# Performance work log

Measured on AMD Instinct MI355X. Metric: run time of the kernel, lower is better.

Reference implementation:

```python
import jax, jax.numpy as jnp
import numpy as np

VOCAB = 32000
D_MODEL = 1024
PATCH_LEN = 16
NHEAD = 8
B = 8
S = 4096


def setup_inputs() -> dict:
    key = jax.random.key(0)
    ks = jax.random.split(key, 8)
    token_inputs = jax.random.randint(ks[0], (B, S), 0, VOCAB, dtype=jnp.int64 if jax.config.jax_enable_x64 else jnp.int32)
    attention_mask = jax.random.randint(ks[1], (B, S), 0, 2).astype(bool)
    emb_weight = jax.random.normal(ks[2], (VOCAB, D_MODEL), dtype=jnp.float32) * 0.02
    patch_query = jax.random.normal(ks[3], (1, 1, D_MODEL), dtype=jnp.float32) * 0.02
    # nn.MultiheadAttention packed in-projection [3D, D] and out projection [D, D]
    lim = 1.0 / np.sqrt(D_MODEL)
    in_proj_w = jax.random.uniform(ks[4], (3 * D_MODEL, D_MODEL), jnp.float32, -lim, lim)
    in_proj_b = jnp.zeros((3 * D_MODEL,), jnp.float32)
    out_w = jax.random.uniform(ks[5], (D_MODEL, D_MODEL), jnp.float32, -lim, lim)
    out_b = jnp.zeros((D_MODEL,), jnp.float32)
    return {
        "token_inputs": token_inputs,
        "attention_mask": attention_mask,
        "emb_weight": emb_weight,
        "patch_query": patch_query,
        "in_proj_w": in_proj_w,
        "in_proj_b": in_proj_b,
        "out_w": out_w,
        "out_b": out_b,
    }


def reference(token_inputs, attention_mask, emb_weight, patch_query, in_proj_w, in_proj_b, out_w, out_b):
    d_model = emb_weight.shape[1]
    h, dh = NHEAD, d_model // NHEAD
    L = PATCH_LEN

    tok_emb = emb_weight[token_inputs]              # [B, S, D]
    bsz, seqlen, _ = tok_emb.shape
    # seqlen chosen divisible by PATCH_LEN -> pad_len == 0 (matches torch path)
    num_patches = seqlen // L
    BP = bsz * num_patches
    patch_tokens = tok_emb.reshape(BP, L, d_model)  # [BP, L, D]
    patch_mask = attention_mask.reshape(BP, L)      # True = valid token

    patch_valid = patch_mask.any(axis=1)            # [BP]
    # force position 0 valid for fully-empty patches (safe softmax)
    safe_mask = patch_mask | ((~patch_valid)[:, None] & (jnp.arange(L) == 0)[None, :])

    wq, wk, wv = jnp.split(in_proj_w, 3, axis=0)    # each [D, D]
    bq, bk, bv = jnp.split(in_proj_b, 3, axis=0)

    q = patch_query[0, 0] @ wq.T + bq               # [D] (same query for all patches)
    k = patch_tokens @ wk.T + bk                    # [BP, L, D]
    v = patch_tokens @ wv.T + bv                    # [BP, L, D]

    qh = q.reshape(h, dh)                           # [H, dh]
    kh = k.reshape(BP, L, h, dh)                    # [BP, L, H, dh]
    vh = v.reshape(BP, L, h, dh)

    scale = 1.0 / jnp.sqrt(jnp.asarray(dh, q.dtype))
    scores = jnp.einsum('hd,blhd->bhl', qh, kh) * scale   # [BP, H, L]
    scores = jnp.where(safe_mask[:, None, :], scores, -jnp.inf)
    attn = jax.nn.softmax(scores, axis=-1)                # [BP, H, L]

    ctx = jnp.einsum('bhl,blhd->bhd', attn, vh).reshape(BP, d_model)
    patch_latent = ctx @ out_w.T + out_b                  # [BP, D]

    patch_latent = patch_latent.reshape(bsz, num_patches, d_model)
    pv = patch_valid.reshape(bsz, num_patches)
    patch_latent = patch_latent * pv[..., None].astype(patch_latent.dtype)
    return patch_latent, pv
```

## Files before the change

### kernel.cpp

```cpp
#include <hip/hip_runtime.h>
#include <stdint.h>

#define OUT_LATENT (2048*1024)
#define SCALE 0.08838834764831845f

typedef float f32x4v __attribute__((ext_vector_type(4)));
typedef short s16x8  __attribute__((ext_vector_type(8)));

static __device__ inline unsigned short f2bf(float f) {
    union { float f; uint32_t u; } v; v.f = f;
    uint32_t u = v.u;
    return (unsigned short)((u + 0x7FFFu + ((u >> 16) & 1u)) >> 16);
}
static __device__ inline float bflo(uint32_t u) {
    union { uint32_t u; float f; } v; v.u = u << 16; return v.f;
}
static __device__ inline float bfhi(uint32_t u) {
    union { uint32_t u; float f; } v; v.u = u & 0xFFFF0000u; return v.f;
}

static __device__ __forceinline__ void async16(const unsigned short* g, unsigned short* l) {
    __builtin_amdgcn_global_load_lds(
        (const __attribute__((address_space(1))) void*)g,
        (__attribute__((address_space(3))) void*)l, 16, 0, 0);
}

__global__ __launch_bounds__(256) void k_convw(
    const float* __restrict__ wv_src, const float* __restrict__ ow_src,
    unsigned short* __restrict__ wv_dst, unsigned short* __restrict__ ow_dst) {
    int t = threadIdx.x, b = blockIdx.x;
    const float* src; unsigned short* dst; int idx;
    if (b < 1024) { src = wv_src; dst = wv_dst; idx = b * 1024 + t * 4; }
    else          { src = ow_src; dst = ow_dst; idx = (b - 1024) * 1024 + t * 4; }
    float4 f = *(const float4*)(src + idx);
    ushort4 o; o.x = f2bf(f.x); o.y = f2bf(f.y); o.z = f2bf(f.z); o.w = f2bf(f.w);
    *(ushort4*)(dst + idx) = o;
}

__global__ __launch_bounds__(256) void k_qvec(
    const float* __restrict__ pq, const float* __restrict__ ipw,
    const float* __restrict__ ipb, float* __restrict__ qv) {
    int t = threadIdx.x, wave = t >> 6, lane = t & 63;
    int d = blockIdx.x * 4 + wave;
    const float* wrow = ipw + (size_t)d * 1024;
    float acc = 0.f;
    #pragma unroll
    for (int i = 0; i < 16; ++i) { int j = lane + i * 64; acc = fmaf(pq[j], wrow[j], acc); }
    #pragma unroll
    for (int m = 32; m >= 1; m >>= 1) acc += __shfl_xor(acc, m);
    if (lane == 0) qv[d] = acc + ipb[d];
}

__global__ __launch_bounds__(256) void k_qk(
    const float* __restrict__ qv, const float* __restrict__ ipw,
    const float* __restrict__ ipb, unsigned short* __restrict__ qkb,
    float* __restrict__ sb) {
    __shared__ float qs[128];
    __shared__ float part[128];
    int h = blockIdx.x, jseg = blockIdx.y, t = threadIdx.x;
    int jl = t & 127, dh = t >> 7;
    if (t < 128) qs[t] = qv[h * 128 + t];
    __syncthreads();
    float acc = 0.f;
    const float* wbase = ipw + (size_t)(1024 + h * 128 + dh * 64) * 1024 + jseg * 128 + jl;
    #pragma unroll 8
    for (int d = 0; d < 64; ++d)
        acc = fmaf(qs[dh * 64 + d], wbase[(size_t)d * 1024], acc);
    if (dh) part[jl] = acc;
    __syncthreads();
    if (!dh) qkb[h * 1024 + jseg * 128 + jl] = f2bf((acc + part[jl]) * SCALE);
    if (jseg == 0 && t < 64) {
        const float* bk = ipb + 1024 + h * 128;
        float p = qs[t] * bk[t] + qs[t + 64] * bk[t + 64];
        #pragma unroll
        for (int m = 32; m >= 1; m >>= 1) p += __shfl_xor(p, m);
        if (t == 0) sb[h] = p * SCALE;
    }
}

__global__ __launch_bounds__(256) void k_attn(
    const int* __restrict__ tok_ids, const int* __restrict__ amask,
    const float* __restrict__ emb, const unsigned short* __restrict__ qkb,
    const float* __restrict__ sb, unsigned short* __restrict__ Mout,
    float* __restrict__ pv) {
    __shared__ unsigned short tokL[16][1032];
    __shared__ float scoresP[4][16][8];
    __shared__ float attnL[16][8];
    __shared__ int allzL;

    int bp = blockIdx.x, t = threadIdx.x;
    int wave = t >> 6, lane = t & 63, lrow = lane & 15, quad = lane >> 4;

    s16x8 bfr[8];
    {
        const unsigned short* qbase = qkb + (lane & 7) * 1024 + wave * 256 + quad * 8;
        #pragma unroll
        for (int s = 0; s < 8; ++s) bfr[s] = *(const s16x8*)(qbase + s * 32);
    }

    {
        int row = t >> 4, c = t & 15;
        int tid = tok_ids[bp * 16 + row];
        const float* erow = emb + (size_t)tid * 1024;
        #pragma unroll
        for (int i = 0; i < 16; ++i) {
            int j4 = c + i * 16;
            float4 f = *(const float4*)(erow + j4 * 4);
            ushort4 o; o.x = f2bf(f.x); o.y = f2bf(f.y); o.z = f2bf(f.z); o.w = f2bf(f.w);
            *(ushort4*)(&tokL[row][j4 * 4]) = o;
        }
    }
    if (t < 16) {
        int any = (amask[bp * 16 + t] != 0);
        any |= __shfl_xor(any, 1); any |= __shfl_xor(any, 2);
        any |= __shfl_xor(any, 4); any |= __shfl_xor(any, 8);
        if (t == 0) { pv[bp] = any ? 1.f : 0.f; allzL = any ? 0 : 1; }
    }
    __syncthreads();

    {
        f32x4v acc = (f32x4v){0.f, 0.f, 0.f, 0.f};
        const unsigned short* arow = &tokL[lrow][wave * 256 + quad * 8];
        #pragma unroll
        for (int s = 0; s < 8; ++s) {
            s16x8 af = *(const s16x8*)(arow + s * 32);
            acc = __builtin_amdgcn_mfma_f32_16x16x32_bf16(af, bfr[s], acc, 0, 0, 0);
        }
        if (lrow < 8) {
            #pragma unroll
            for (int r = 0; r < 4; ++r) scoresP[wave][quad * 4 + r][lrow] = acc[r];
        }
    }
    __syncthreads();

    if (t < 128) {
        int hh = t >> 4, ll = t & 15;
        float s = scoresP[0][ll][hh] + scoresP[1][ll][hh]
                + scoresP[2][ll][hh] + scoresP[3][ll][hh] + sb[hh];
        bool valid = (amask[bp * 16 + ll] != 0) || (allzL && ll == 0);
        s = valid ? s : -1e30f;
        float mx = s;
        mx = fmaxf(mx, __shfl_xor(mx, 1)); mx = fmaxf(mx, __shfl_xor(mx, 2));
        mx = fmaxf(mx, __shfl_xor(mx, 4)); mx = fmaxf(mx, __shfl_xor(mx, 8));
        float e = __expf(s - mx);
        float sum = e;
        sum += __shfl_xor(sum, 1); sum += __shfl_xor(sum, 2);
        sum += __shfl_xor(sum, 4); sum += __shfl_xor(sum, 8);
        attnL[ll][hh] = e / sum;
    }
    __syncthreads();

    float macc[8][4];
    #pragma unroll
    for (int h = 0; h < 8; ++h)
        #pragma unroll
        for (int c = 0; c < 4; ++c) macc[h][c] = 0.f;
    #pragma unroll
    for (int ll = 0; ll < 16; ++ll) {
        uint2 tv = *(const uint2*)(&tokL[ll][t * 4]);
        float t0 = bflo(tv.x), t1 = bfhi(tv.x), t2 = bflo(tv.y), t3 = bfhi(tv.y);
        float4 a0 = *(const float4*)(&attnL[ll][0]);
        float4 a1 = *(const float4*)(&attnL[ll][4]);
        macc[0][0] = fmaf(a0.x, t0, macc[0][0]); macc[0][1] = fmaf(a0.x, t1, macc[0][1]);
        macc[0][2] = fmaf(a0.x, t2, macc[0][2]); macc[0][3] = fmaf(a0.x, t3, macc[0][3]);
        macc[1][0] = fmaf(a0.y, t0, macc[1][0]); macc[1][1] = fmaf(a0.y, t1, macc[1][1]);
        macc[1][2] = fmaf(a0.y, t2, macc[1][2]); macc[1][3] = fmaf(a0.y, t3, macc[1][3]);
        macc[2][0] = fmaf(a0.z, t0, macc[2][0]); macc[2][1] = fmaf(a0.z, t1, macc[2][1]);
        macc[2][2] = fmaf(a0.z, t2, macc[2][2]); macc[2][3] = fmaf(a0.z, t3, macc[2][3]);
        macc[3][0] = fmaf(a0.w, t0, macc[3][0]); macc[3][1] = fmaf(a0.w, t1, macc[3][1]);
        macc[3][2] = fmaf(a0.w, t2, macc[3][2]); macc[3][3] = fmaf(a0.w, t3, macc[3][3]);
        macc[4][0] = fmaf(a1.x, t0, macc[4][0]); macc[4][1] = fmaf(a1.x, t1, macc[4][1]);
        macc[4][2] = fmaf(a1.x, t2, macc[4][2]); macc[4][3] = fmaf(a1.x, t3, macc[4][3]);
        macc[5][0] = fmaf(a1.y, t0, macc[5][0]); macc[5][1] = fmaf(a1.y, t1, macc[5][1]);
        macc[5][2] = fmaf(a1.y, t2, macc[5][2]); macc[5][3] = fmaf(a1.y, t3, macc[5][3]);
        macc[6][0] = fmaf(a1.z, t0, macc[6][0]); macc[6][1] = fmaf(a1.z, t1, macc[6][1]);
        macc[6][2] = fmaf(a1.z, t2, macc[6][2]); macc[6][3] = fmaf(a1.z, t3, macc[6][3]);
        macc[7][0] = fmaf(a1.w, t0, macc[7][0]); macc[7][1] = fmaf(a1.w, t1, macc[7][1]);
        macc[7][2] = fmaf(a1.w, t2, macc[7][2]); macc[7][3] = fmaf(a1.w, t3, macc[7][3]);
    }
    #pragma unroll
    for (int h = 0; h < 8; ++h) {
        ushort4 o;
        o.x = f2bf(macc[h][0]); o.y = f2bf(macc[h][1]);
        o.z = f2bf(macc[h][2]); o.w = f2bf(macc[h][3]);
        *(ushort4*)(Mout + ((size_t)(h * 2048 + bp)) * 1024 + t * 4) = o;
    }
}

__device__ __forceinline__ void gemm128_mainloop(
    const unsigned short* __restrict__ A, const unsigned short* __restrict__ B,
    unsigned short* As, unsigned short* Bs, f32x4v acc[4][4]) {
    int t = threadIdx.x;
    int wave = t >> 6, lane = t & 63, lrow = lane & 15, quad = lane >> 4;
    int wm = wave & 1, wn = wave >> 1;
    int srow = t >> 2, sseg = (t & 3) * 8;
    #pragma unroll
    for (int mi = 0; mi < 4; ++mi)
        #pragma unroll
        for (int ni = 0; ni < 4; ++ni) acc[mi][ni] = (f32x4v){0.f, 0.f, 0.f, 0.f};
    for (int step = 0; step < 32; ++step) {
        int k0 = step * 32;
        __syncthreads();
        async16(A + (size_t)srow * 1024 + k0 + sseg,        As + t * 8);
        async16(A + (size_t)(srow + 64) * 1024 + k0 + sseg, As + (256 + t) * 8);
        async16(B + (size_t)srow * 1024 + k0 + sseg,        Bs + t * 8);
        async16(B + (size_t)(srow + 64) * 1024 + k0 + sseg, Bs + (256 + t) * 8);
        __syncthreads();
        s16x8 af[4], bf[4];
        #pragma unroll
        for (int i = 0; i < 4; ++i) {
            af[i] = *(const s16x8*)(As + (wm * 64 + i * 16 + lrow) * 32 + quad * 8);
            bf[i] = *(const s16x8*)(Bs + (wn * 64 + i * 16 + lrow) * 32 + quad * 8);
        }
        #pragma unroll
        for (int mi = 0; mi < 4; ++mi)
            #pragma unroll
            for (int ni = 0; ni < 4; ++ni)
                acc[mi][ni] = __builtin_amdgcn_mfma_f32_16x16x32_bf16(af[mi], bf[ni], acc[mi][ni], 0, 0, 0);
    }
}

__global__ __launch_bounds__(256) void k_gemm_ctx(
    const unsigned short* __restrict__ M, const unsigned short* __restrict__ wv,
    const float* __restrict__ ipb, unsigned short* __restrict__ ctx) {
    __shared__ unsigned short As[128 * 32], Bs[128 * 32];
    int mb = blockIdx.x, h = blockIdx.y;
    f32x4v acc[4][4];
    gemm128_mainloop(M + ((size_t)h * 2048 + mb * 128) * 1024,
                     wv + (size_t)h * 128 * 1024, As, Bs, acc);
    int t = threadIdx.x, wave = t >> 6, lane = t & 63, lrow = lane & 15, quad = lane >> 4;
    int wm = wave & 1, wn = wave >> 1;
    #pragma unroll
    for (int ni = 0; ni < 4; ++ni) {
        int n_g = h * 128 + wn * 64 + ni * 16 + lrow;
        float bias = ipb[2048 + n_g];
        #pragma unroll
        for (int mi = 0; mi < 4; ++mi) {
            #pragma unroll
            for (int r = 0; r < 4; ++r) {
                int m_g = mb * 128 + wm * 64 + mi * 16 + quad * 4 + r;
                ctx[(size_t)m_g * 1024 + n_g] = f2bf(acc[mi][ni][r] + bias);
            }
        }
    }
}

__global__ __launch_bounds__(256) void k_gemm_out(
    const unsigned short* __restrict__ ctx, const unsigned short* __restrict__ ow,
    const float* __restrict__ outb, const float* __restrict__ pv,
    float* __restrict__ out) {
    __shared__ unsigned short As[128 * 32], Bs[128 * 32];
    int mb = blockIdx.x, nb = blockIdx.y;
    f32x4v acc[4][4];
    gemm128_mainloop(ctx + (size_t)mb * 128 * 1024,
                     ow + (size_t)nb * 128 * 1024, As, Bs, acc);
    int t = threadIdx.x, wave = t >> 6, lane = t & 63, lrow = lane & 15, quad = lane >> 4;
    int wm = wave & 1, wn = wave >> 1;
    #pragma unroll
    for (int ni = 0; ni < 4; ++ni) {
        int n_g = nb * 128 + wn * 64 + ni * 16 + lrow;
        float bias = outb[n_g];
        #pragma unroll
        for (int mi = 0; mi < 4; ++mi) {
            #pragma unroll
            for (int r = 0; r < 4; ++r) {
                int m_g = mb * 128 + wm * 64 + mi * 16 + quad * 4 + r;
                out[(size_t)m_g * 1024 + n_g] = (acc[mi][ni][r] + bias) * pv[m_g];
            }
        }
    }
    if (nb == 0 && t < 128) out[OUT_LATENT + mb * 128 + t] = pv[mb * 128 + t];
}

extern "C" void kernel_launch(void* const* d_in, const int* in_sizes, int n_in,
                              void* d_out, int out_size, void* d_ws, size_t ws_size,
                              hipStream_t stream) {
    const int*   tok = (const int*)d_in[0];
    const int*   msk = (const int*)d_in[1];
    const float* emb = (const float*)d_in[2];
    const float* pq  = (const float*)d_in[3];
    const float* ipw = (const float*)d_in[4];
    const float* ipb = (const float*)d_in[5];
    const float* ow  = (const float*)d_in[6];
    const float* ob  = (const float*)d_in[7];
    float* out = (float*)d_out;
    char* ws = (char*)d_ws;

    float*          q_f   = (float*)(ws + 0);
    float*          sb_f  = (float*)(ws + 4096);
    float*          pv_f  = (float*)(ws + 8192);
    unsigned short* qk_b  = (unsigned short*)(ws + 16384);
    unsigned short* wv_b  = (unsigned short*)(ws + 32768);
    unsigned short* ow_b  = (unsigned short*)(ws + 32768 + 2097152);
    unsigned short* ctx_b = (unsigned short*)(ws + 32768 + 2 * 2097152);
    unsigned short* M_b   = (unsigned short*)(ws + 32768 + 2 * 2097152 + 4194304);

    k_convw<<<dim3(2048), dim3(256), 0, stream>>>(ipw + (size_t)2048 * 1024, ow, wv_b, ow_b);
    k_qvec <<<dim3(256),  dim3(256), 0, stream>>>(pq, ipw, ipb, q_f);
    k_qk   <<<dim3(8, 8), dim3(256), 0, stream>>>(q_f, ipw, ipb, qk_b, sb_f);
    k_attn <<<dim3(2048), dim3(256), 0, stream>>>(tok, msk, emb, qk_b, sb_f, M_b, pv_f);
    k_gemm_ctx<<<dim3(16, 8), dim3(256), 0, stream>>>(M_b, wv_b, ipb, ctx_b);
    k_gemm_out<<<dim3(16, 8), dim3(256), 0, stream>>>(ctx_b, ow_b, ob, pv_f, out);
}
```

Baseline: 268.5 us.

## Double-buffer GEMM mainloop, fold weight conversion into attention launch, split qk wider

After: 263.5 us. About the same (-1.9%).

```diff
diff --git a/kernel.cpp b/kernel.cpp
--- a/kernel.cpp
+++ b/kernel.cpp
@@ -23,18 +23,6 @@
     __builtin_amdgcn_global_load_lds(
         (const __attribute__((address_space(1))) void*)g,
         (__attribute__((address_space(3))) void*)l, 16, 0, 0);
-}
-
-__global__ __launch_bounds__(256) void k_convw(
-    const float* __restrict__ wv_src, const float* __restrict__ ow_src,
-    unsigned short* __restrict__ wv_dst, unsigned short* __restrict__ ow_dst) {
-    int t = threadIdx.x, b = blockIdx.x;
-    const float* src; unsigned short* dst; int idx;
-    if (b < 1024) { src = wv_src; dst = wv_dst; idx = b * 1024 + t * 4; }
-    else          { src = ow_src; dst = ow_dst; idx = (b - 1024) * 1024 + t * 4; }
-    float4 f = *(const float4*)(src + idx);
-    ushort4 o; o.x = f2bf(f.x); o.y = f2bf(f.y); o.z = f2bf(f.z); o.w = f2bf(f.w);
-    *(ushort4*)(dst + idx) = o;
 }
 
 __global__ __launch_bounds__(256) void k_qvec(
@@ -56,19 +44,20 @@
     const float* __restrict__ ipb, unsigned short* __restrict__ qkb,
     float* __restrict__ sb) {
     __shared__ float qs[128];
-    __shared__ float part[128];
+    __shared__ float part[3][64];
     int h = blockIdx.x, jseg = blockIdx.y, t = threadIdx.x;
-    int jl = t & 127, dh = t >> 7;
+    int jl = t & 63, dh = t >> 6;
     if (t < 128) qs[t] = qv[h * 128 + t];
     __syncthreads();
     float acc = 0.f;
-    const float* wbase = ipw + (size_t)(1024 + h * 128 + dh * 64) * 1024 + jseg * 128 + jl;
+    const float* wbase = ipw + (size_t)(1024 + h * 128 + dh * 32) * 1024 + jseg * 64 + jl;
     #pragma unroll 8
-    for (int d = 0; d < 64; ++d)
-        acc = fmaf(qs[dh * 64 + d], wbase[(size_t)d * 1024], acc);
-    if (dh) part[jl] = acc;
-    __syncthreads();
-    if (!dh) qkb[h * 1024 + jseg * 128 + jl] = f2bf((acc + part[jl]) * SCALE);
+    for (int d = 0; d < 32; ++d)
+        acc = fmaf(qs[dh * 32 + d], wbase[(size_t)d * 1024], acc);
+    if (dh) part[dh - 1][jl] = acc;
+    __syncthreads();
+    if (!dh) qkb[h * 1024 + jseg * 64 + jl] =
+        f2bf((acc + part[0][jl] + part[1][jl] + part[2][jl]) * SCALE);
     if (jseg == 0 && t < 64) {
         const float* bk = ipb + 1024 + h * 128;
         float p = qs[t] * bk[t] + qs[t + 64] * bk[t + 64];
@@ -78,15 +67,28 @@
     }
 }
 
-__global__ __launch_bounds__(256) void k_attn(
+__global__ __launch_bounds__(256) void k_attn_conv(
     const int* __restrict__ tok_ids, const int* __restrict__ amask,
     const float* __restrict__ emb, const unsigned short* __restrict__ qkb,
     const float* __restrict__ sb, unsigned short* __restrict__ Mout,
-    float* __restrict__ pv) {
+    float* __restrict__ pv,
+    const float* __restrict__ wv_src, const float* __restrict__ ow_src,
+    unsigned short* __restrict__ wv_dst, unsigned short* __restrict__ ow_dst) {
     __shared__ unsigned short tokL[16][1032];
     __shared__ float scoresP[4][16][8];
     __shared__ float attnL[16][8];
     __shared__ int allzL;
+
+    if (blockIdx.x >= 2048) {
+        int b = blockIdx.x - 2048, t = threadIdx.x;
+        const float* src; unsigned short* dst; int idx;
+        if (b < 1024) { src = wv_src; dst = wv_dst; idx = b * 1024 + t * 4; }
+        else          { src = ow_src; dst = ow_dst; idx = (b - 1024) * 1024 + t * 4; }
+        float4 f = *(const float4*)(src + idx);
+        ushort4 o; o.x = f2bf(f.x); o.y = f2bf(f.y); o.z = f2bf(f.z); o.w = f2bf(f.w);
+        *(ushort4*)(dst + idx) = o;
+        return;
+    }
 
     int bp = blockIdx.x, t = threadIdx.x;
     int wave = t >> 6, lane = t & 63, lrow = lane & 15, quad = lane >> 4;
@@ -194,36 +196,55 @@
     int wave = t >> 6, lane = t & 63, lrow = lane & 15, quad = lane >> 4;
     int wm = wave & 1, wn = wave >> 1;
     int srow = t >> 2, sseg = (t & 3) * 8;
+    size_t a0 = (size_t)srow * 1024 + sseg;
+    size_t a1 = (size_t)(srow + 64) * 1024 + sseg;
     #pragma unroll
     for (int mi = 0; mi < 4; ++mi)
         #pragma unroll
         for (int ni = 0; ni < 4; ++ni) acc[mi][ni] = (f32x4v){0.f, 0.f, 0.f, 0.f};
-    for (int step = 0; step < 32; ++step) {
-        int k0 = step * 32;
+
+    auto stage = [&](int step, int buf) {
+        int k0 = step * 64;
+        unsigned short* as = As + buf * 8192;
+        unsigned short* bs = Bs + buf * 8192;
+        #pragma unroll
+        for (int ks = 0; ks < 2; ++ks) {
+            async16(A + a0 + k0 + ks * 32, as + ks * 4096 + t * 8);
+            async16(A + a1 + k0 + ks * 32, as + ks * 4096 + (256 + t) * 8);
+            async16(B + a0 + k0 + ks * 32, bs + ks * 4096 + t * 8);
+            async16(B + a1 + k0 + ks * 32, bs + ks * 4096 + (256 + t) * 8);
+        }
+    };
+
+    stage(0, 0);
+    __syncthreads();
+    for (int s = 0; s < 16; ++s) {
+        int cur = s & 1;
+        if (s + 1 < 16) stage(s + 1, cur ^ 1);
+        const unsigned short* as = As + cur * 8192;
+        const unsigned short* bs = Bs + cur * 8192;
+        #pragma unroll
+        for (int ks = 0; ks < 2; ++ks) {
+            s16x8 af[4], bf[4];
+            #pragma unroll
+            for (int i = 0; i < 4; ++i) {
+                af[i] = *(const s16x8*)(as + ks * 4096 + (wm * 64 + i * 16 + lrow) * 32 + quad * 8);
+                bf[i] = *(const s16x8*)(bs + ks * 4096 + (wn * 64 + i * 16 + lrow) * 32 + quad * 8);
+            }
+            #pragma unroll
+            for (int mi = 0; mi < 4; ++mi)
+                #pragma unroll
+                for (int ni = 0; ni < 4; ++ni)
+                    acc[mi][ni] = __builtin_amdgcn_mfma_f32_16x16x32_bf16(af[mi], bf[ni], acc[mi][ni], 0, 0, 0);
+        }
         __syncthreads();
-        async16(A + (size_t)srow * 1024 + k0 + sseg,        As + t * 8);
-        async16(A + (size_t)(srow + 64) * 1024 + k0 + sseg, As + (256 + t) * 8);
-        async16(B + (size_t)srow * 1024 + k0 + sseg,        Bs + t * 8);
-        async16(B + (size_t)(srow + 64) * 1024 + k0 + sseg, Bs + (256 + t) * 8);
-        __syncthreads();
-        s16x8 af[4], bf[4];
-        #pragma unroll
-        for (int i = 0; i < 4; ++i) {
-            af[i] = *(const s16x8*)(As + (wm * 64 + i * 16 + lrow) * 32 + quad * 8);
-            bf[i] = *(const s16x8*)(Bs + (wn * 64 + i * 16 + lrow) * 32 + quad * 8);
-        }
-        #pragma unroll
-        for (int mi = 0; mi < 4; ++mi)
-            #pragma unroll
-            for (int ni = 0; ni < 4; ++ni)
-                acc[mi][ni] = __builtin_amdgcn_mfma_f32_16x16x32_bf16(af[mi], bf[ni], acc[mi][ni], 0, 0, 0);
     }
 }
 
 __global__ __launch_bounds__(256) void k_gemm_ctx(
     const unsigned short* __restrict__ M, const unsigned short* __restrict__ wv,
     const float* __restrict__ ipb, unsigned short* __restrict__ ctx) {
-    __shared__ unsigned short As[128 * 32], Bs[128 * 32];
+    __shared__ unsigned short As[2 * 8192], Bs[2 * 8192];
     int mb = blockIdx.x, h = blockIdx.y;
     f32x4v acc[4][4];
     gemm128_mainloop(M + ((size_t)h * 2048 + mb * 128) * 1024,
@@ -249,7 +270,7 @@
     const unsigned short* __restrict__ ctx, const unsigned short* __restrict__ ow,
     const float* __restrict__ outb, const float* __restrict__ pv,
     float* __restrict__ out) {
-    __shared__ unsigned short As[128 * 32], Bs[128 * 32];
+    __shared__ unsigned short As[2 * 8192], Bs[2 * 8192];
     int mb = blockIdx.x, nb = blockIdx.y;
     f32x4v acc[4][4];
     gemm128_mainloop(ctx + (size_t)mb * 128 * 1024,
@@ -295,10 +316,11 @@
     unsigned short* ctx_b = (unsigned short*)(ws + 32768 + 2 * 2097152);
     unsigned short* M_b   = (unsigned short*)(ws + 32768 + 2 * 2097152 + 4194304);
 
-    k_convw<<<dim3(2048), dim3(256), 0, stream>>>(ipw + (size_t)2048 * 1024, ow, wv_b, ow_b);
-    k_qvec <<<dim3(256),  dim3(256), 0, stream>>>(pq, ipw, ipb, q_f);
-    k_qk   <<<dim3(8, 8), dim3(256), 0, stream>>>(q_f, ipw, ipb, qk_b, sb_f);
-    k_attn <<<dim3(2048), dim3(256), 0, stream>>>(tok, msk, emb, qk_b, sb_f, M_b, pv_f);
+    k_qvec <<<dim3(256),   dim3(256), 0, stream>>>(pq, ipw, ipb, q_f);
+    k_qk   <<<dim3(8, 16), dim3(256), 0, stream>>>(q_f, ipw, ipb, qk_b, sb_f);
+    k_attn_conv<<<dim3(4096), dim3(256), 0, stream>>>(
+        tok, msk, emb, qk_b, sb_f, M_b, pv_f,
+        ipw + (size_t)2048 * 1024, ow, wv_b, ow_b);
     k_gemm_ctx<<<dim3(16, 8), dim3(256), 0, stream>>>(M_b, wv_b, ipb, ctx_b);
     k_gemm_out<<<dim3(16, 8), dim3(256), 0, stream>>>(ctx_b, ow_b, ob, pv_f, out);
 }
```
